# Kernel tuning notes

Hardware: AMD Instinct MI355X
Metric: run time of the kernel (lower is better)

## Reference

```python
import jax, jax.numpy as jnp
import numpy as np

N = 20000          # nodes
E = 320000         # edges (before self-loops)
H, C = 8, 32       # heads, hidden_size
ND, ED = 6, 11     # node_dim, edge_dim (hard-coded in module)
HC = H * C
DIFF_SCALE = 100.0
SLOPE = 0.2        # GATv2 leaky_relu negative_slope


def _glorot(k, shape):
    fan_in, fan_out = shape[0], shape[-1]
    lim = float(np.sqrt(6.0 / (fan_in + fan_out)))
    return jax.random.uniform(k, shape, jnp.float32, -lim, lim)


def setup_inputs() -> dict:
    key = jax.random.key(0)
    ks = jax.random.split(key, 16)
    d = {}
    d["x"] = jax.random.normal(ks[0], (N, ND), jnp.float32)
    d["edge_index"] = jax.random.randint(ks[1], (2, E), 0, N)
    d["edge_attr"] = jax.random.normal(ks[2], (E, ED), jnp.float32)
    # layer 0 (node_dim -> H*C, with edge features)
    d["Wl0"] = _glorot(ks[3], (ND, HC)); d["bl0"] = jnp.zeros((HC,), jnp.float32)
    d["Wr0"] = _glorot(ks[4], (ND, HC)); d["br0"] = jnp.zeros((HC,), jnp.float32)
    d["We0"] = _glorot(ks[5], (ED, HC))
    d["att0"] = _glorot(ks[6], (H, C))
    d["bias0"] = jnp.zeros((HC,), jnp.float32)
    # layer 1 (H*C -> H*C, no edge features)
    d["Wl1"] = _glorot(ks[7], (HC, HC)); d["bl1"] = jnp.zeros((HC,), jnp.float32)
    d["Wr1"] = _glorot(ks[8], (HC, HC)); d["br1"] = jnp.zeros((HC,), jnp.float32)
    d["att1"] = _glorot(ks[9], (H, C))
    d["bias1"] = jnp.zeros((HC,), jnp.float32)
    return d


def _gatv2(x, src, tgt, Wl, bl, Wr, br, att, bias, e=None, We=None):
    n = x.shape[0]
    xl = (x @ Wl + bl).reshape(n, H, C)   # source transform (messages)
    xr = (x @ Wr + br).reshape(n, H, C)   # target transform
    m = xl[src] + xr[tgt]                 # [E', H, C]
    if e is not None:
        m = m + (e @ We).reshape(-1, H, C)
    s = jax.nn.leaky_relu(m, SLOPE)
    logits = jnp.einsum('ehc,hc->eh', s, att)            # [E', H]
    # segment softmax over incoming edges of each target node
    mx = jax.ops.segment_max(logits, tgt, num_segments=n)
    ex = jnp.exp(logits - mx[tgt])
    den = jax.ops.segment_sum(ex, tgt, num_segments=n)
    alpha = ex / den[tgt]                                 # [E', H]
    out = jax.ops.segment_sum(alpha[:, :, None] * xl[src], tgt, num_segments=n)
    return out.reshape(n, HC) + bias


def reference(x, edge_index, edge_attr, Wl0, bl0, Wr0, br0, We0, att0, bias0,
              Wl1, bl1, Wr1, br1, att1, bias1):
    # preprocessing from GraphEmbedder.forward
    x = jnp.where((x[:, 2] == 1)[:, None] & (jnp.arange(ND) == 1)[None, :],
                  ((x[:, 1] - x[:, 0]) / DIFF_SCALE)[:, None], x)
    edge_attr = jnp.where((edge_attr[:, -2] == 1)[:, None] & (jnp.arange(ED) == 1)[None, :],
                          ((edge_attr[:, 1] - edge_attr[:, 0]) / DIFF_SCALE)[:, None], edge_attr)
    # add self-loops (PyG GATv2Conv default, fill_value='mean' for edge_attr)
    loop = jnp.arange(N)
    src = jnp.concatenate([edge_index[0], loop])
    tgt = jnp.concatenate([edge_index[1], loop])
    ea = jnp.concatenate([edge_attr, jnp.broadcast_to(edge_attr.mean(0), (N, ED))])
    h = _gatv2(x, src, tgt, Wl0, bl0, Wr0, br0, att0, bias0, e=ea, We=We0)
    h = jax.nn.elu(h)
    h = _gatv2(h, src, tgt, Wl1, bl1, Wr1, br1, att1, bias1)
    return h
```

## Files before the change

kernel.cpp:

```cpp
#include <hip/hip_runtime.h>
#include <cstddef>

#define N_H 8
#define N_C 32
#define N_HC 256
#define SLOPE 0.2f

typedef __attribute__((ext_vector_type(8))) short short8v;
typedef __attribute__((ext_vector_type(4))) float f32x4;

__device__ __forceinline__ short f2bf(float f) {
    unsigned u = __float_as_uint(f);
    unsigned r = (u + 0x7FFFu + ((u >> 16) & 1u)) >> 16;
    return (short)r;
}
__device__ __forceinline__ float bf2f(short s) {
    return __uint_as_float(((unsigned)(unsigned short)s) << 16);
}

__global__ __launch_bounds__(256) void edge_prep_kernel(const int* __restrict__ ei,
                                                        const float* __restrict__ ea,
                                                        int* __restrict__ deg,
                                                        float* __restrict__ sums, int E,
                                                        int Etot) {
    float loc[11];
#pragma unroll
    for (int j = 0; j < 11; ++j) loc[j] = 0.f;
    for (int i = blockIdx.x * blockDim.x + threadIdx.x; i < Etot; i += gridDim.x * blockDim.x) {
        int t = (i < E) ? ei[E + i] : i - E;
        atomicAdd(&deg[t], 1);
        if (i < E) {
            float r[11];
#pragma unroll
            for (int j = 0; j < 11; ++j) r[j] = ea[(size_t)i * 11 + j];
            if (r[9] == 1.0f) r[1] = (r[1] - r[0]) * 0.01f;
#pragma unroll
            for (int j = 0; j < 11; ++j) loc[j] += r[j];
        }
    }
    __shared__ float sbuf[256];
#pragma unroll
    for (int j = 0; j < 11; ++j) {
        sbuf[threadIdx.x] = loc[j];
        __syncthreads();
        for (int s = 128; s > 0; s >>= 1) {
            if (threadIdx.x < s) sbuf[threadIdx.x] += sbuf[threadIdx.x + s];
            __syncthreads();
        }
        if (threadIdx.x == 0) atomicAdd(&sums[j], sbuf[0]);
        __syncthreads();
    }
}

__global__ __launch_bounds__(1024) void scan_kernel(const int* __restrict__ deg,
                                                    int* __restrict__ offs,
                                                    int* __restrict__ cursor,
                                                    const float* __restrict__ sums,
                                                    float* __restrict__ mean, int Nn, int E) {
    const int T = 1024;
    int tid = threadIdx.x;
    if (tid < 11) mean[tid] = sums[tid] / (float)E;
    int chunk = (Nn + T - 1) / T;
    int b = tid * chunk;
    int s = 0;
    for (int k = 0; k < chunk; ++k) {
        int i = b + k;
        if (i < Nn) s += deg[i];
    }
    __shared__ int sm[T];
    sm[tid] = s;
    __syncthreads();
    for (int d = 1; d < T; d <<= 1) {
        int v = (tid >= d) ? sm[tid - d] : 0;
        __syncthreads();
        sm[tid] += v;
        __syncthreads();
    }
    int pref = (tid > 0) ? sm[tid - 1] : 0;
    for (int k = 0; k < chunk; ++k) {
        int i = b + k;
        if (i < Nn) {
            offs[i] = pref;
            cursor[i] = pref;
            pref += deg[i];
        }
    }
    if (tid == T - 1) offs[Nn] = sm[T - 1];
}

__global__ __launch_bounds__(256) void scatter_kernel(const int* __restrict__ ei,
                                                      const float* __restrict__ ea,
                                                      const float* __restrict__ mean_ea,
                                                      int* __restrict__ cursor,
                                                      int* __restrict__ esrc,
                                                      float* __restrict__ ea_csr, int E,
                                                      int Etot) {
    int e = blockIdx.x * blockDim.x + threadIdx.x;
    if (e >= Etot) return;
    int s, t;
    if (e < E) { s = ei[e]; t = ei[E + e]; }
    else       { s = t = e - E; }
    int pos = atomicAdd(&cursor[t], 1);
    esrc[pos] = s;
    float r[11];
    if (e < E) {
#pragma unroll
        for (int j = 0; j < 11; ++j) r[j] = ea[(size_t)e * 11 + j];
        if (r[9] == 1.0f) r[1] = (r[1] - r[0]) * 0.01f;
    } else {
#pragma unroll
        for (int j = 0; j < 11; ++j) r[j] = mean_ea[j];
    }
    float* dst = ea_csr + (size_t)pos * 12;
#pragma unroll
    for (int j = 0; j < 11; ++j) dst[j] = r[j];
}

template <int K, int R>
__global__ __launch_bounds__(256) void node_mm_kernel(const float* __restrict__ X,
                                                      const float* __restrict__ Wl,
                                                      const float* __restrict__ bl,
                                                      const float* __restrict__ Wr,
                                                      const float* __restrict__ br,
                                                      float* __restrict__ xl,
                                                      float* __restrict__ xr, int Nn) {
    __shared__ float xs[R][K];
    int row0 = blockIdx.x * R;
    int tid = threadIdx.x;
    for (int i = tid; i < R * K; i += blockDim.x) {
        int r = i / K, k = i - r * K;
        int gr = row0 + r;
        float v = 0.f;
        if (gr < Nn) {
            v = X[(size_t)gr * K + k];
            if (k == 1) {
                float x0 = X[(size_t)gr * K + 0];
                float x2 = X[(size_t)gr * K + 2];
                if (x2 == 1.0f) v = (v - x0) * 0.01f;
            }
        }
        xs[r][k] = v;
    }
    __syncthreads();
    int c = tid;
    float accl[R], accr[R];
#pragma unroll
    for (int r = 0; r < R; ++r) { accl[r] = bl[c]; accr[r] = br[c]; }
#pragma unroll
    for (int k = 0; k < K; ++k) {
        float wl = Wl[k * N_HC + c], wr = Wr[k * N_HC + c];
#pragma unroll
        for (int r = 0; r < R; ++r) {
            accl[r] = fmaf(xs[r][k], wl, accl[r]);
            accr[r] = fmaf(xs[r][k], wr, accr[r]);
        }
    }
#pragma unroll
    for (int r = 0; r < R; ++r) {
        int gr = row0 + r;
        if (gr < Nn) {
            xl[(size_t)gr * N_HC + c] = accl[r];
            xr[(size_t)gr * N_HC + c] = accr[r];
        }
    }
}

__global__ __launch_bounds__(256) void convert_w_kernel(const float* __restrict__ Wl,
                                                        const float* __restrict__ Wr,
                                                        short* __restrict__ Bfhi,
                                                        short* __restrict__ Bflo) {
    int n = blockIdx.x;
    int k = threadIdx.x;
    float v = (n < 256) ? Wl[(size_t)k * 256 + n] : Wr[(size_t)k * 256 + (n - 256)];
    short hi = f2bf(v);
    short lo = f2bf(v - bf2f(hi));
    int cg = n >> 6, ni = (n >> 4) & 3, lm = n & 15;
    int k0 = k >> 5, lg = (k >> 3) & 3, e = k & 7;
    int lane = lg * 16 + lm;
    size_t idx = ((((size_t)cg * 8 + k0) * 4 + ni) * 64 + lane) * 8 + e;
    Bfhi[idx] = hi;
    Bflo[idx] = lo;
}

__global__ __launch_bounds__(256) void gemm_mfma_kernel(
    const short* __restrict__ Ahi, const short* __restrict__ Alo,
    const short* __restrict__ Bfhi, const short* __restrict__ Bflo,
    const float* __restrict__ bl, const float* __restrict__ br, float* __restrict__ xl,
    float* __restrict__ xr, int Nn) {
    const int wid = threadIdx.x >> 6, lane = threadIdx.x & 63;
    const int lm = lane & 15, lg = lane >> 4;
    const int r0 = blockIdx.x * 16;
    const int half = blockIdx.y;
    const int cg = half * 4 + wid;
    const int kg = lg * 8;

    f32x4 acc0 = {0.f, 0.f, 0.f, 0.f}, acc1 = acc0, acc2 = acc0, acc3 = acc0;

    const int rA = r0 + lm;
    const bool va = rA < Nn;
    const short* pah = Ahi + (size_t)rA * 256 + kg;
    const short* pal = Alo + (size_t)rA * 256 + kg;
    const short8v zz = (short8v)0;

#pragma unroll 2
    for (int ks = 0; ks < 8; ++ks) {
        const int k0 = ks * 32;
        short8v ah = va ? *(const short8v*)(pah + k0) : zz;
        short8v al = va ? *(const short8v*)(pal + k0) : zz;
        const size_t fb = (((size_t)cg * 8 + ks) * 4) * 512 + (size_t)lane * 8;
        const short8v bh0 = *(const short8v*)(Bfhi + fb + 0 * 512);
        const short8v bl0 = *(const short8v*)(Bflo + fb + 0 * 512);
        const short8v bh1 = *(const short8v*)(Bfhi + fb + 1 * 512);
        const short8v bl1 = *(const short8v*)(Bflo + fb + 1 * 512);
        const short8v bh2 = *(const short8v*)(Bfhi + fb + 2 * 512);
        const short8v bl2 = *(const short8v*)(Bflo + fb + 2 * 512);
        const short8v bh3 = *(const short8v*)(Bfhi + fb + 3 * 512);
        const short8v bl3 = *(const short8v*)(Bflo + fb + 3 * 512);
        acc0 = __builtin_amdgcn_mfma_f32_16x16x32_bf16(ah, bh0, acc0, 0, 0, 0);
        acc0 = __builtin_amdgcn_mfma_f32_16x16x32_bf16(al, bh0, acc0, 0, 0, 0);
        acc0 = __builtin_amdgcn_mfma_f32_16x16x32_bf16(ah, bl0, acc0, 0, 0, 0);
        acc1 = __builtin_amdgcn_mfma_f32_16x16x32_bf16(ah, bh1, acc1, 0, 0, 0);
        acc1 = __builtin_amdgcn_mfma_f32_16x16x32_bf16(al, bh1, acc1, 0, 0, 0);
        acc1 = __builtin_amdgcn_mfma_f32_16x16x32_bf16(ah, bl1, acc1, 0, 0, 0);
        acc2 = __builtin_amdgcn_mfma_f32_16x16x32_bf16(ah, bh2, acc2, 0, 0, 0);
        acc2 = __builtin_amdgcn_mfma_f32_16x16x32_bf16(al, bh2, acc2, 0, 0, 0);
        acc2 = __builtin_amdgcn_mfma_f32_16x16x32_bf16(ah, bl2, acc2, 0, 0, 0);
        acc3 = __builtin_amdgcn_mfma_f32_16x16x32_bf16(ah, bh3, acc3, 0, 0, 0);
        acc3 = __builtin_amdgcn_mfma_f32_16x16x32_bf16(al, bh3, acc3, 0, 0, 0);
        acc3 = __builtin_amdgcn_mfma_f32_16x16x32_bf16(ah, bl3, acc3, 0, 0, 0);
    }

    const float* __restrict__ bias = half ? br : bl;
    float* __restrict__ dst = half ? xr : xl;
    const int clbase = wid * 64 + lm;
#pragma unroll
    for (int ni = 0; ni < 4; ++ni) {
        int col = clbase + ni * 16;
        float bv = bias[col];
        f32x4 a = (ni == 0) ? acc0 : (ni == 1) ? acc1 : (ni == 2) ? acc2 : acc3;
        int rb = r0 + lg * 4;
#pragma unroll
        for (int e = 0; e < 4; ++e) {
            int row = rb + e;
            if (row < Nn) dst[(size_t)row * N_HC + col] = a[e] + bv;
        }
    }
}

__device__ __forceinline__ void online_update(float logit, const float4& xlv, float& m,
                                              float& den, float4& acc) {
    float mn = fmaxf(m, logit);
    float s = __expf(m - mn);
    float w = __expf(logit - mn);
    den = den * s + w;
    acc.x = fmaf(w, xlv.x, acc.x * s);
    acc.y = fmaf(w, xlv.y, acc.y * s);
    acc.z = fmaf(w, xlv.z, acc.z * s);
    acc.w = fmaf(w, xlv.w, acc.w * s);
    m = mn;
}

template <bool L0>
__device__ __forceinline__ float edge_logit(const float4& xlv, const float4& xrv,
                                            const float4* Wreg, const float* __restrict__ eap,
                                            const float4& av) {
    float m0 = xlv.x + xrv.x, m1 = xlv.y + xrv.y, m2 = xlv.z + xrv.z, m3 = xlv.w + xrv.w;
    if (L0) {
#pragma unroll
        for (int j = 0; j < 11; ++j) {
            float aj = eap[j];
            m0 = fmaf(aj, Wreg[j].x, m0);
            m1 = fmaf(aj, Wreg[j].y, m1);
            m2 = fmaf(aj, Wreg[j].z, m2);
            m3 = fmaf(aj, Wreg[j].w, m3);
        }
    }
    m0 = m0 > 0.f ? m0 : SLOPE * m0;
    m1 = m1 > 0.f ? m1 : SLOPE * m1;
    m2 = m2 > 0.f ? m2 : SLOPE * m2;
    m3 = m3 > 0.f ? m3 : SLOPE * m3;
    float p = m0 * av.x + m1 * av.y + m2 * av.z + m3 * av.w;
    p += __shfl_xor(p, 1);
    p += __shfl_xor(p, 2);
    p += __shfl_xor(p, 4);
    return p;
}

template <bool L0>
__global__ __launch_bounds__(256) void node_gather_kernel(
    const int* __restrict__ offs, const int* __restrict__ esrc,
    const float* __restrict__ ea_csr, const float* __restrict__ We,
    const float* __restrict__ att, const float* __restrict__ xl, const float* __restrict__ xr,
    const float* __restrict__ bias, float* __restrict__ out, short* __restrict__ oAhi,
    short* __restrict__ oAlo, int Nn) {
    int wid = threadIdx.x >> 6;
    int lane = threadIdx.x & 63;
    int node = blockIdx.x * 4 + wid;
    if (node >= Nn) return;
    int c4 = lane * 4;

    float4 Wreg[11];
    if (L0) {
#pragma unroll
        for (int j = 0; j < 11; ++j) Wreg[j] = *(const float4*)(We + j * N_HC + c4);
    }
    const float4 xrv = *(const float4*)(xr + (size_t)node * N_HC + c4);
    const float4 av = *(const float4*)(att + c4);

    int beg = offs[node], end = offs[node + 1];

    float mA = -INFINITY, dA = 0.f;
    float mB = -INFINITY, dB = 0.f;
    float mC = -INFINITY, dC = 0.f;
    float mD = -INFINITY, dD = 0.f;
    float4 aA = {0.f, 0.f, 0.f, 0.f}, aB = aA, aC = aA, aD = aA;

    int p = beg;
    for (; p + 3 < end; p += 4) {
        int pu = __builtin_amdgcn_readfirstlane(p);
        int s0 = esrc[pu + 0];
        int s1 = esrc[pu + 1];
        int s2 = esrc[pu + 2];
        int s3 = esrc[pu + 3];
        const float4 x0 = *(const float4*)(xl + (size_t)s0 * N_HC + c4);
        const float4 x1 = *(const float4*)(xl + (size_t)s1 * N_HC + c4);
        const float4 x2 = *(const float4*)(xl + (size_t)s2 * N_HC + c4);
        const float4 x3 = *(const float4*)(xl + (size_t)s3 * N_HC + c4);
        const float* e0 = L0 ? (ea_csr + (size_t)(pu + 0) * 12) : nullptr;
        const float* e1 = L0 ? (ea_csr + (size_t)(pu + 1) * 12) : nullptr;
        const float* e2 = L0 ? (ea_csr + (size_t)(pu + 2) * 12) : nullptr;
        const float* e3 = L0 ? (ea_csr + (size_t)(pu + 3) * 12) : nullptr;
        float lg0 = edge_logit<L0>(x0, xrv, Wreg, e0, av);
        float lg1 = edge_logit<L0>(x1, xrv, Wreg, e1, av);
        float lg2 = edge_logit<L0>(x2, xrv, Wreg, e2, av);
        float lg3 = edge_logit<L0>(x3, xrv, Wreg, e3, av);
        online_update(lg0, x0, mA, dA, aA);
        online_update(lg1, x1, mB, dB, aB);
        online_update(lg2, x2, mC, dC, aC);
        online_update(lg3, x3, mD, dD, aD);
    }
    for (; p < end; ++p) {
        int pu = __builtin_amdgcn_readfirstlane(p);
        int s0 = esrc[pu];
        const float4 x0 = *(const float4*)(xl + (size_t)s0 * N_HC + c4);
        const float* e0 = L0 ? (ea_csr + (size_t)pu * 12) : nullptr;
        float lg0 = edge_logit<L0>(x0, xrv, Wreg, e0, av);
        online_update(lg0, x0, mA, dA, aA);
    }

    float mm = fmaxf(fmaxf(mA, mB), fmaxf(mC, mD));
    float sA = __expf(mA - mm), sB = __expf(mB - mm);
    float sC = __expf(mC - mm), sD = __expf(mD - mm);
    float den = dA * sA + dB * sB + dC * sC + dD * sD;
    float4 acct;
    acct.x = aA.x * sA + aB.x * sB + aC.x * sC + aD.x * sD;
    acct.y = aA.y * sA + aB.y * sB + aC.y * sC + aD.y * sD;
    acct.z = aA.z * sA + aB.z * sB + aC.z * sC + aD.z * sD;
    acct.w = aA.w * sA + aB.w * sB + aC.w * sC + aD.w * sD;

    const float4 bv = *(const float4*)(bias + c4);
    float4 r;
    r.x = acct.x / den + bv.x;
    r.y = acct.y / den + bv.y;
    r.z = acct.z / den + bv.z;
    r.w = acct.w / den + bv.w;
    if (L0) {
        r.x = r.x > 0.f ? r.x : (__expf(r.x) - 1.f);
        r.y = r.y > 0.f ? r.y : (__expf(r.y) - 1.f);
        r.z = r.z > 0.f ? r.z : (__expf(r.z) - 1.f);
        r.w = r.w > 0.f ? r.w : (__expf(r.w) - 1.f);
    }
    if (oAhi) {
        short h0 = f2bf(r.x), h1 = f2bf(r.y), h2 = f2bf(r.z), h3 = f2bf(r.w);
        short4 hv = {h0, h1, h2, h3};
        short4 lv = {f2bf(r.x - bf2f(h0)), f2bf(r.y - bf2f(h1)), f2bf(r.z - bf2f(h2)),
                     f2bf(r.w - bf2f(h3))};
        *(short4*)(oAhi + (size_t)node * N_HC + c4) = hv;
        *(short4*)(oAlo + (size_t)node * N_HC + c4) = lv;
    } else {
        *(float4*)(out + (size_t)node * N_HC + c4) = r;
    }
}

extern "C" void kernel_launch(void* const* d_in, const int* in_sizes, int n_in, void* d_out,
                              int out_size, void* d_ws, size_t ws_size, hipStream_t stream) {
    const float* x = (const float*)d_in[0];
    const int* ei = (const int*)d_in[1];
    const float* ea = (const float*)d_in[2];
    const float* Wl0 = (const float*)d_in[3];
    const float* bl0 = (const float*)d_in[4];
    const float* Wr0 = (const float*)d_in[5];
    const float* br0 = (const float*)d_in[6];
    const float* We0 = (const float*)d_in[7];
    const float* att0 = (const float*)d_in[8];
    const float* bias0 = (const float*)d_in[9];
    const float* Wl1 = (const float*)d_in[10];
    const float* bl1 = (const float*)d_in[11];
    const float* Wr1 = (const float*)d_in[12];
    const float* br1 = (const float*)d_in[13];
    const float* att1 = (const float*)d_in[14];
    const float* bias1 = (const float*)d_in[15];
    float* out = (float*)d_out;

    const int Nn = in_sizes[0] / 6;
    const int E = in_sizes[1] / 2;
    const int Etot = E + Nn;

    auto align16 = [](size_t v) { return (v + 15) & ~(size_t)15; };
    float* ws = (float*)d_ws;
    size_t o = 0;
    float* xl = ws + o;     o = align16(o + (size_t)Nn * N_HC);
    float* xr = ws + o;     o = align16(o + (size_t)Nn * N_HC);
    float* h = ws + o;      o = align16(o + (size_t)Nn * N_HC);
    float* ea_csr = ws + o; o = align16(o + (size_t)Etot * 12);
    float* easum = ws + o;  o = align16(o + 16);
    float* mean = ws + o;   o = align16(o + 16);
    int* deg = (int*)(ws + o);    o = align16(o + (size_t)Nn);
    int* offs = (int*)(ws + o);   o = align16(o + (size_t)Nn + 1);
    int* cursor = (int*)(ws + o); o = align16(o + (size_t)Nn);
    int* esrc = (int*)(ws + o);   o = align16(o + (size_t)Etot);
    short* Bfhi = (short*)(ws + o); o = align16(o + 512 * 256 / 2);
    short* Bflo = (short*)(ws + o); o = align16(o + 512 * 256 / 2);
    const bool use_mfma = (o * sizeof(float) <= ws_size);

    hipMemsetAsync(easum, 0, 16 * sizeof(float), stream);
    hipMemsetAsync(deg, 0, (size_t)Nn * sizeof(int), stream);

    edge_prep_kernel<<<512, 256, 0, stream>>>(ei, ea, deg, easum, E, Etot);
    scan_kernel<<<1, 1024, 0, stream>>>(deg, offs, cursor, easum, mean, Nn, E);
    scatter_kernel<<<(Etot + 255) / 256, 256, 0, stream>>>(ei, ea, mean, cursor, esrc, ea_csr, E,
                                                           Etot);

    const int gblocks = (Nn + 3) / 4;

    short* Ahi = (short*)d_out;
    short* Alo = Ahi + (size_t)Nn * N_HC;

    node_mm_kernel<6, 8><<<(Nn + 7) / 8, 256, 0, stream>>>(x, Wl0, bl0, Wr0, br0, xl, xr, Nn);
    node_gather_kernel<true><<<gblocks, 256, 0, stream>>>(offs, esrc, ea_csr, We0, att0, xl, xr,
                                                          bias0, h, use_mfma ? Ahi : nullptr,
                                                          use_mfma ? Alo : nullptr, Nn);

    if (use_mfma) {
        convert_w_kernel<<<512, 256, 0, stream>>>(Wl1, Wr1, Bfhi, Bflo);
        dim3 mgrid((Nn + 15) / 16, 2);
        gemm_mfma_kernel<<<mgrid, 256, 0, stream>>>(Ahi, Alo, Bfhi, Bflo, bl1, br1, xl, xr, Nn);
    } else {
        dim3 ggrid((Nn + 127) / 128, 4);
        node_mm_kernel<256, 8><<<(Nn + 7) / 8, 256, 0, stream>>>(h, Wl1, bl1, Wr1, br1, xl, xr,
                                                                 Nn);
    }
    node_gather_kernel<false><<<gblocks, 256, 0, stream>>>(offs, esrc, nullptr, nullptr, att1, xl,
                                                           xr, bias1, out, nullptr, nullptr, Nn);
}
```

Before: 325.9 us.

## Stage edge attributes in original order and gather them by edge index

Edge attributes are now preprocessed once, in original edge order, into a padded 12-float buffer with coalesced float4 loads through shared memory. The mean row for self-loops is appended at index E. The scatter kernel now writes only an edge-index permutation instead of copying 11 floats per edge into CSR order. The degree histogram moves to its own kernel. This removes the scattered 11-float writes in the scatter stage, but the layer-0 gather gains an extra indirection and non-contiguous reads of edge attributes.

```diff
diff --git a/kernel.cpp b/kernel.cpp
--- a/kernel.cpp
+++ b/kernel.cpp
@@ -18,48 +18,71 @@
     return __uint_as_float(((unsigned)(unsigned short)s) << 16);
 }
 
-__global__ __launch_bounds__(256) void edge_prep_kernel(const int* __restrict__ ei,
-                                                        const float* __restrict__ ea,
-                                                        int* __restrict__ deg,
-                                                        float* __restrict__ sums, int E,
-                                                        int Etot) {
+__global__ __launch_bounds__(256) void ea_stage_kernel(const float* __restrict__ ea,
+                                                       float* __restrict__ eap,
+                                                       float* __restrict__ sums, int E) {
+    __shared__ float s1[256 * 11];
+    __shared__ float sbuf[256];
+    const int tid = threadIdx.x;
+    const int base = blockIdx.x * 256;
+    const int cnt = min(256, E - base);
+    const int nfl = cnt * 11;
+    const int nf4 = nfl >> 2;
+    for (int j = tid; j < nf4; j += 256) {
+        float4 v = *(const float4*)(ea + (size_t)base * 11 + (size_t)j * 4);
+        s1[j * 4 + 0] = v.x;
+        s1[j * 4 + 1] = v.y;
+        s1[j * 4 + 2] = v.z;
+        s1[j * 4 + 3] = v.w;
+    }
+    for (int j = nf4 * 4 + tid; j < nfl; j += 256) s1[j] = ea[(size_t)base * 11 + j];
+    __syncthreads();
+
     float loc[11];
 #pragma unroll
     for (int j = 0; j < 11; ++j) loc[j] = 0.f;
-    for (int i = blockIdx.x * blockDim.x + threadIdx.x; i < Etot; i += gridDim.x * blockDim.x) {
-        int t = (i < E) ? ei[E + i] : i - E;
-        atomicAdd(&deg[t], 1);
-        if (i < E) {
-            float r[11];
-#pragma unroll
-            for (int j = 0; j < 11; ++j) r[j] = ea[(size_t)i * 11 + j];
-            if (r[9] == 1.0f) r[1] = (r[1] - r[0]) * 0.01f;
-#pragma unroll
-            for (int j = 0; j < 11; ++j) loc[j] += r[j];
-        }
-    }
-    __shared__ float sbuf[256];
+    if (tid < cnt) {
+        float r[11];
+#pragma unroll
+        for (int j = 0; j < 11; ++j) r[j] = s1[tid * 11 + j];
+        if (r[9] == 1.0f) r[1] = (r[1] - r[0]) * 0.01f;
+#pragma unroll
+        for (int j = 0; j < 11; ++j) loc[j] += r[j];
+        float4* dst = (float4*)(eap + (size_t)(base + tid) * 12);
+        dst[0] = {r[0], r[1], r[2], r[3]};
+        dst[1] = {r[4], r[5], r[6], r[7]};
+        dst[2] = {r[8], r[9], r[10], 0.f};
+    }
+
 #pragma unroll
     for (int j = 0; j < 11; ++j) {
-        sbuf[threadIdx.x] = loc[j];
+        sbuf[tid] = loc[j];
         __syncthreads();
         for (int s = 128; s > 0; s >>= 1) {
-            if (threadIdx.x < s) sbuf[threadIdx.x] += sbuf[threadIdx.x + s];
+            if (tid < s) sbuf[tid] += sbuf[tid + s];
             __syncthreads();
         }
-        if (threadIdx.x == 0) atomicAdd(&sums[j], sbuf[0]);
+        if (tid == 0) atomicAdd(&sums[j], sbuf[0]);
         __syncthreads();
     }
+}
+
+__global__ __launch_bounds__(256) void deg_hist_kernel(const int* __restrict__ ei,
+                                                       int* __restrict__ deg, int E, int Etot) {
+    int e = blockIdx.x * blockDim.x + threadIdx.x;
+    if (e >= Etot) return;
+    int t = (e < E) ? ei[E + e] : e - E;
+    atomicAdd(&deg[t], 1);
 }
 
 __global__ __launch_bounds__(1024) void scan_kernel(const int* __restrict__ deg,
                                                     int* __restrict__ offs,
                                                     int* __restrict__ cursor,
                                                     const float* __restrict__ sums,
-                                                    float* __restrict__ mean, int Nn, int E) {
+                                                    float* __restrict__ eap, int Nn, int E) {
     const int T = 1024;
     int tid = threadIdx.x;
-    if (tid < 11) mean[tid] = sums[tid] / (float)E;
+    if (tid < 12) eap[(size_t)E * 12 + tid] = (tid < 11) ? sums[tid] / (float)E : 0.f;
     int chunk = (Nn + T - 1) / T;
     int b = tid * chunk;
     int s = 0;
@@ -89,12 +112,9 @@
 }
 
 __global__ __launch_bounds__(256) void scatter_kernel(const int* __restrict__ ei,
-                                                      const float* __restrict__ ea,
-                                                      const float* __restrict__ mean_ea,
                                                       int* __restrict__ cursor,
                                                       int* __restrict__ esrc,
-                                                      float* __restrict__ ea_csr, int E,
-                                                      int Etot) {
+                                                      int* __restrict__ eidx, int E, int Etot) {
     int e = blockIdx.x * blockDim.x + threadIdx.x;
     if (e >= Etot) return;
     int s, t;
@@ -102,18 +122,7 @@
     else       { s = t = e - E; }
     int pos = atomicAdd(&cursor[t], 1);
     esrc[pos] = s;
-    float r[11];
-    if (e < E) {
-#pragma unroll
-        for (int j = 0; j < 11; ++j) r[j] = ea[(size_t)e * 11 + j];
-        if (r[9] == 1.0f) r[1] = (r[1] - r[0]) * 0.01f;
-    } else {
-#pragma unroll
-        for (int j = 0; j < 11; ++j) r[j] = mean_ea[j];
-    }
-    float* dst = ea_csr + (size_t)pos * 12;
-#pragma unroll
-    for (int j = 0; j < 11; ++j) dst[j] = r[j];
+    eidx[pos] = (e < E) ? e : E;
 }
 
 template <int K, int R>
@@ -288,8 +297,8 @@
 
 template <bool L0>
 __global__ __launch_bounds__(256) void node_gather_kernel(
-    const int* __restrict__ offs, const int* __restrict__ esrc,
-    const float* __restrict__ ea_csr, const float* __restrict__ We,
+    const int* __restrict__ offs, const int* __restrict__ esrc, const int* __restrict__ eidx,
+    const float* __restrict__ eap, const float* __restrict__ We,
     const float* __restrict__ att, const float* __restrict__ xl, const float* __restrict__ xr,
     const float* __restrict__ bias, float* __restrict__ out, short* __restrict__ oAhi,
     short* __restrict__ oAlo, int Nn) {
@@ -326,10 +335,13 @@
         const float4 x1 = *(const float4*)(xl + (size_t)s1 * N_HC + c4);
         const float4 x2 = *(const float4*)(xl + (size_t)s2 * N_HC + c4);
         const float4 x3 = *(const float4*)(xl + (size_t)s3 * N_HC + c4);
-        const float* e0 = L0 ? (ea_csr + (size_t)(pu + 0) * 12) : nullptr;
-        const float* e1 = L0 ? (ea_csr + (size_t)(pu + 1) * 12) : nullptr;
-        const float* e2 = L0 ? (ea_csr + (size_t)(pu + 2) * 12) : nullptr;
-        const float* e3 = L0 ? (ea_csr + (size_t)(pu + 3) * 12) : nullptr;
+        const float *e0 = nullptr, *e1 = nullptr, *e2 = nullptr, *e3 = nullptr;
+        if (L0) {
+            e0 = eap + (size_t)eidx[pu + 0] * 12;
+            e1 = eap + (size_t)eidx[pu + 1] * 12;
+            e2 = eap + (size_t)eidx[pu + 2] * 12;
+            e3 = eap + (size_t)eidx[pu + 3] * 12;
+        }
         float lg0 = edge_logit<L0>(x0, xrv, Wreg, e0, av);
         float lg1 = edge_logit<L0>(x1, xrv, Wreg, e1, av);
         float lg2 = edge_logit<L0>(x2, xrv, Wreg, e2, av);
@@ -343,7 +355,7 @@
         int pu = __builtin_amdgcn_readfirstlane(p);
         int s0 = esrc[pu];
         const float4 x0 = *(const float4*)(xl + (size_t)s0 * N_HC + c4);
-        const float* e0 = L0 ? (ea_csr + (size_t)pu * 12) : nullptr;
+        const float* e0 = L0 ? (eap + (size_t)eidx[pu] * 12) : nullptr;
         float lg0 = edge_logit<L0>(x0, xrv, Wreg, e0, av);
         online_update(lg0, x0, mA, dA, aA);
     }
@@ -409,16 +421,16 @@
     auto align16 = [](size_t v) { return (v + 15) & ~(size_t)15; };
     float* ws = (float*)d_ws;
     size_t o = 0;
-    float* xl = ws + o;     o = align16(o + (size_t)Nn * N_HC);
-    float* xr = ws + o;     o = align16(o + (size_t)Nn * N_HC);
-    float* h = ws + o;      o = align16(o + (size_t)Nn * N_HC);
-    float* ea_csr = ws + o; o = align16(o + (size_t)Etot * 12);
-    float* easum = ws + o;  o = align16(o + 16);
-    float* mean = ws + o;   o = align16(o + 16);
+    float* xl = ws + o;    o = align16(o + (size_t)Nn * N_HC);
+    float* xr = ws + o;    o = align16(o + (size_t)Nn * N_HC);
+    float* h = ws + o;     o = align16(o + (size_t)Nn * N_HC);
+    float* eap = ws + o;   o = align16(o + (size_t)(E + 1) * 12);
+    float* easum = ws + o; o = align16(o + 16);
     int* deg = (int*)(ws + o);    o = align16(o + (size_t)Nn);
     int* offs = (int*)(ws + o);   o = align16(o + (size_t)Nn + 1);
     int* cursor = (int*)(ws + o); o = align16(o + (size_t)Nn);
     int* esrc = (int*)(ws + o);   o = align16(o + (size_t)Etot);
+    int* eidx = (int*)(ws + o);   o = align16(o + (size_t)Etot);
     short* Bfhi = (short*)(ws + o); o = align16(o + 512 * 256 / 2);
     short* Bflo = (short*)(ws + o); o = align16(o + 512 * 256 / 2);
     const bool use_mfma = (o * sizeof(float) <= ws_size);
@@ -426,10 +438,10 @@
     hipMemsetAsync(easum, 0, 16 * sizeof(float), stream);
     hipMemsetAsync(deg, 0, (size_t)Nn * sizeof(int), stream);
 
-    edge_prep_kernel<<<512, 256, 0, stream>>>(ei, ea, deg, easum, E, Etot);
-    scan_kernel<<<1, 1024, 0, stream>>>(deg, offs, cursor, easum, mean, Nn, E);
-    scatter_kernel<<<(Etot + 255) / 256, 256, 0, stream>>>(ei, ea, mean, cursor, esrc, ea_csr, E,
-                                                           Etot);
+    ea_stage_kernel<<<(E + 255) / 256, 256, 0, stream>>>(ea, eap, easum, E);
+    deg_hist_kernel<<<(Etot + 255) / 256, 256, 0, stream>>>(ei, deg, E, Etot);
+    scan_kernel<<<1, 1024, 0, stream>>>(deg, offs, cursor, easum, eap, Nn, E);
+    scatter_kernel<<<(Etot + 255) / 256, 256, 0, stream>>>(ei, cursor, esrc, eidx, E, Etot);
 
     const int gblocks = (Nn + 3) / 4;
 
@@ -437,8 +449,8 @@
     short* Alo = Ahi + (size_t)Nn * N_HC;
 
     node_mm_kernel<6, 8><<<(Nn + 7) / 8, 256, 0, stream>>>(x, Wl0, bl0, Wr0, br0, xl, xr, Nn);
-    node_gather_kernel<true><<<gblocks, 256, 0, stream>>>(offs, esrc, ea_csr, We0, att0, xl, xr,
-                                                          bias0, h, use_mfma ? Ahi : nullptr,
+    node_gather_kernel<true><<<gblocks, 256, 0, stream>>>(offs, esrc, eidx, eap, We0, att0, xl,
+                                                          xr, bias0, h, use_mfma ? Ahi : nullptr,
                                                           use_mfma ? Alo : nullptr, Nn);
 
     if (use_mfma) {
@@ -446,10 +458,10 @@
         dim3 mgrid((Nn + 15) / 16, 2);
         gemm_mfma_kernel<<<mgrid, 256, 0, stream>>>(Ahi, Alo, Bfhi, Bflo, bl1, br1, xl, xr, Nn);
     } else {
-        dim3 ggrid((Nn + 127) / 128, 4);
         node_mm_kernel<256, 8><<<(Nn + 7) / 8, 256, 0, stream>>>(h, Wl1, bl1, Wr1, br1, xl, xr,
                                                                  Nn);
     }
-    node_gather_kernel<false><<<gblocks, 256, 0, stream>>>(offs, esrc, nullptr, nullptr, att1, xl,
-                                                           xr, bias1, out, nullptr, nullptr, Nn);
-}
+    node_gather_kernel<false><<<gblocks, 256, 0, stream>>>(offs, esrc, nullptr, nullptr, nullptr,
+                                                           att1, xl, xr, bias1, out, nullptr,
+                                                           nullptr, Nn);
+}
```

Measured after the change: 436.6 us. 1.34x slower.
